# Performance work log

Hardware: AMD Instinct MI355X
Metric: run time of the kernel (lower is better)

## Reference

```python
import math
import jax, jax.numpy as jnp
import numpy as np

B, N, DIM = 2, 4096, 768
H, DK, DV = 8, 64, 64


def setup_inputs() -> dict:
    key = jax.random.key(0)
    ks = jax.random.split(key, 6)
    s = 0.02
    return {
        "x": jax.random.normal(ks[0], (B, N, DIM), dtype=jnp.float32),
        "Wq": jax.random.normal(ks[1], (DIM, H * DK), dtype=jnp.float32) * s,
        "Wk": jax.random.normal(ks[2], (DIM, H * DK), dtype=jnp.float32) * s,
        "Wv": jax.random.normal(ks[3], (DIM, H * DV), dtype=jnp.float32) * s,
        "Wo": jax.random.normal(ks[4], (H * DV, DIM), dtype=jnp.float32) * s,
        "bo": jax.random.normal(ks[5], (DIM,), dtype=jnp.float32) * s,
    }


def reference(x, Wq, Wk, Wv, Wo, bo):
    b, n, _ = x.shape
    # project and split heads: [B, H, N, d]
    q = (x @ Wq).reshape(b, n, H, DK).transpose(0, 2, 1, 3)
    k = (x @ Wk).reshape(b, n, H, DK).transpose(0, 2, 1, 3)
    v = (x @ Wv).reshape(b, n, H, DV).transpose(0, 2, 1, 3)
    scale = 1.0 / math.sqrt(DK)
    scores = jnp.einsum("bhnd,bhmd->bhnm", q, k) * scale  # [B,H,N,N]
    attn = jax.nn.softmax(scores, axis=-1)
    out = jnp.einsum("bhnm,bhmd->bhnd", attn, v)  # [B,H,N,DV]
    out = out.transpose(0, 2, 1, 3).reshape(b, n, H * DV)
    return out @ Wo + bo
```

## Files before the change

### kernel.cpp

```cpp
#include <hip/hip_runtime.h>
#include <hip/hip_bf16.h>

#define B_   2
#define N_   4096
#define DIM_ 768
#define H_   8
#define MROWS_ 8192

typedef __bf16 bf16x8 __attribute__((ext_vector_type(8)));
typedef __bf16 bf16x4 __attribute__((ext_vector_type(4)));
typedef float  f32x4  __attribute__((ext_vector_type(4)));

static __device__ __forceinline__ f32x4 mfma16(bf16x8 a, bf16x8 b, f32x4 c) {
    return __builtin_amdgcn_mfma_f32_16x16x32_bf16(a, b, c, 0, 0, 0);
}

#define GLDS16(g, l) \
    __builtin_amdgcn_global_load_lds((const __attribute__((address_space(1))) void*)(g), \
                                     (__attribute__((address_space(3))) void*)(l), 16, 0, 0)

__global__ void cvt_x_kernel(const float* __restrict__ x, __bf16* __restrict__ xb, int n4) {
    int i = blockIdx.x * blockDim.x + threadIdx.x;
    if (i >= n4) return;
    float4 f = reinterpret_cast<const float4*>(x)[i];
    bf16x4 o;
    o[0] = (__bf16)f.x; o[1] = (__bf16)f.y; o[2] = (__bf16)f.z; o[3] = (__bf16)f.w;
    reinterpret_cast<bf16x4*>(xb)[i] = o;
}

__global__ __launch_bounds__(256) void transpose_w_kernel(const float* __restrict__ Wq,
                                                          const float* __restrict__ Wk,
                                                          const float* __restrict__ Wv,
                                                          const float* __restrict__ Wo,
                                                          __bf16* __restrict__ wt,
                                                          __bf16* __restrict__ wot) {
    __shared__ float tile[64][65];
    const int bix = blockIdx.x;
    const float* src;
    int src_ld, rbase, cbase, dst_ld, drow, dcol;
    __bf16* dst;
    if (bix < 288) {
        int m = bix / 96, t = bix - m * 96;
        int tr = t >> 3, tc = t & 7;
        src = (m == 0) ? Wq : ((m == 1) ? Wk : Wv);
        src_ld = 512; rbase = tr * 64; cbase = tc * 64;
        dst = wt; dst_ld = 768; drow = m * 512 + tc * 64; dcol = tr * 64;
    } else {
        int t = bix - 288;
        int tr = t / 12, tc = t - tr * 12;
        src = Wo; src_ld = 768; rbase = tr * 64; cbase = tc * 64;
        dst = wot; dst_ld = 512; drow = tc * 64; dcol = tr * 64;
    }
#pragma unroll
    for (int kk = 0; kk < 4; ++kk) {
        int idx = threadIdx.x + kk * 256;
        int r = idx >> 4, c = (idx & 15) << 2;
        float4 f = *reinterpret_cast<const float4*>(&src[(size_t)(rbase + r) * src_ld + cbase + c]);
        tile[r][c] = f.x; tile[r][c + 1] = f.y; tile[r][c + 2] = f.z; tile[r][c + 3] = f.w;
    }
    __syncthreads();
#pragma unroll
    for (int kk = 0; kk < 4; ++kk) {
        int idx = threadIdx.x + kk * 256;
        int r = idx >> 4, c = (idx & 15) << 2;
        bf16x4 ov;
        ov[0] = (__bf16)tile[c][r];     ov[1] = (__bf16)tile[c + 1][r];
        ov[2] = (__bf16)tile[c + 2][r]; ov[3] = (__bf16)tile[c + 3][r];
        *reinterpret_cast<bf16x4*>(&dst[(size_t)(drow + r) * dst_ld + dcol + c]) = ov;
    }
}

template<int KSTEPS>
__device__ __forceinline__ void gemm_tile_main(const __bf16* __restrict__ A, const int lda,
                                               const int arow0,
                                               const __bf16* __restrict__ Bt, const int ldb,
                                               const int bcol0,
                                               __bf16* __restrict__ abuf,
                                               __bf16* __restrict__ bbuf,
                                               f32x4 (&acc)[4][4]) {
    const int lane = threadIdx.x & 63, wave = threadIdx.x >> 6;
    const int lr = lane & 15, lg = lane >> 4;
    const int wr = wave >> 1, wc = wave & 1;

    const int cid0 = wave * 128 + lane;
    const int cid1 = cid0 + 64;
    const __bf16* sA0 = A  + (size_t)(arow0 + (cid0 >> 2)) * lda + (cid0 & 3) * 8;
    const __bf16* sA1 = A  + (size_t)(arow0 + (cid1 >> 2)) * lda + (cid1 & 3) * 8;
    const __bf16* sB0 = Bt + (size_t)(bcol0 + (cid0 >> 2)) * ldb + (cid0 & 3) * 8;
    const __bf16* sB1 = Bt + (size_t)(bcol0 + (cid1 >> 2)) * ldb + (cid1 & 3) * 8;

    auto stage = [&](int buf, int ks) {
        __bf16* da = abuf + buf * 4096 + wave * 1024;
        __bf16* db = bbuf + buf * 4096 + wave * 1024;
        GLDS16(sA0 + ks * 32, da);
        GLDS16(sA1 + ks * 32, da + 512);
        GLDS16(sB0 + ks * 32, db);
        GLDS16(sB1 + ks * 32, db + 512);
    };

    stage(0, 0);
    asm volatile("s_waitcnt vmcnt(0)" ::: "memory");
    __syncthreads();

    const int ar_off = (wr * 64 + lr) * 32 + lg * 8;
    const int br_off = (wc * 64 + lr) * 32 + lg * 8;

    int buf = 0;
    for (int ks = 0; ks < KSTEPS; ++ks) {
        if (ks + 1 < KSTEPS) stage(buf ^ 1, ks + 1);
        const __bf16* ab = abuf + buf * 4096 + ar_off;
        const __bf16* bb = bbuf + buf * 4096 + br_off;
        bf16x8 af[4], bfr[4];
#pragma unroll
        for (int m = 0; m < 4; ++m) af[m] = *reinterpret_cast<const bf16x8*>(ab + m * 512);
#pragma unroll
        for (int n = 0; n < 4; ++n) bfr[n] = *reinterpret_cast<const bf16x8*>(bb + n * 512);
#pragma unroll
        for (int m = 0; m < 4; ++m)
#pragma unroll
            for (int n = 0; n < 4; ++n)
                acc[m][n] = mfma16(af[m], bfr[n], acc[m][n]);
        asm volatile("s_waitcnt vmcnt(0)" ::: "memory");
        __syncthreads();
        buf ^= 1;
    }
}

__global__ __launch_bounds__(256) void qkv_gemm_kernel(const __bf16* __restrict__ xb,
                                                       const __bf16* __restrict__ wt,
                                                       __bf16* __restrict__ q,
                                                       __bf16* __restrict__ k,
                                                       __bf16* __restrict__ vt) {
    __shared__ __align__(16) __bf16 abuf[2 * 4096];
    __shared__ __align__(16) __bf16 bbuf[2 * 4096];

    const int bid = blockIdx.x;
    const int vb = (bid & 7) * 96 + (bid >> 3);
    const int by = vb % 12, bx = vb / 12;

    f32x4 acc[4][4] = {};
    gemm_tile_main<24>(xb, 768, bx * 128, wt, 768, by * 128, abuf, bbuf, acc);

    const int lane = threadIdx.x & 63, wave = threadIdx.x >> 6;
    const int lr = lane & 15, lg = lane >> 4;
    const int wr = wave >> 1, wc = wave & 1;
    const int bi = (bx * 128) >> 12;
    const int nbase = (bx * 128) & 4095;

    const float QSCALE = 0.125f * 1.44269504089f;

#pragma unroll
    for (int n = 0; n < 4; ++n) {
        const int col0 = by * 128 + wc * 64 + n * 16;
        const int mtx = col0 >> 9;
        const int h   = (col0 >> 6) & 7;
        const int d0  = (col0 & 63) + lr;
        const size_t hb = (size_t)(bi * 8 + h);
#pragma unroll
        for (int m = 0; m < 4; ++m) {
            const int nn = nbase + wr * 64 + m * 16 + lg * 4;
            if (mtx == 0) {
#pragma unroll
                for (int r = 0; r < 4; ++r)
                    q[(hb * 4096 + nn + r) * 64 + d0] = (__bf16)(acc[m][n][r] * QSCALE);
            } else if (mtx == 1) {
#pragma unroll
                for (int r = 0; r < 4; ++r)
                    k[(hb * 4096 + nn + r) * 64 + d0] = (__bf16)acc[m][n][r];
            } else {
                bf16x4 ov;
#pragma unroll
                for (int r = 0; r < 4; ++r) ov[r] = (__bf16)acc[m][n][r];
                *reinterpret_cast<bf16x4*>(&vt[(hb * 64 + d0) * 4096 + nn]) = ov;
            }
        }
    }
}

__global__ __launch_bounds__(256) void attn_kernel(const __bf16* __restrict__ q,
                                                   const __bf16* __restrict__ k,
                                                   const __bf16* __restrict__ vt,
                                                   __bf16* __restrict__ o) {
    const int lane = threadIdx.x & 63, wave = threadIdx.x >> 6;
    const int lr = lane & 15, lg = lane >> 4;

    const int bid  = blockIdx.x;
    const int vbid = (bid & 7) * 64 + (bid >> 3);
    const int qtile = vbid & 31;
    const int bh    = vbid >> 5;
    const int qbase = qtile * 128 + wave * 32;

    const __bf16* Qh = q  + (size_t)bh * N_ * 64;
    const __bf16* Kh = k  + (size_t)bh * N_ * 64;
    const __bf16* Vh = vt + (size_t)bh * 64 * N_;

    __shared__ __align__(16) __bf16 kbuf[2][2][64][64];
    __shared__ __align__(16) __bf16 vbuf[2][2][64][64];
    __bf16* kb0 = &kbuf[0][0][0][0];
    __bf16* vb0 = &vbuf[0][0][0][0];

    const int l8 = lane >> 3, l7 = lane & 7;
    const int swz8 = (l7 ^ l8) * 8;

    int ksrc[4];
#pragma unroll
    for (int c = 0; c < 4; ++c) {
        int i = (wave & 1) * 32 + c * 8 + l8;
        int sig = ((i >> 4) & 1) * 32 + ((i >> 2) & 3) * 8 + ((i >> 5) & 1) * 4 + (i & 3);
        ksrc[c] = sig * 64 + swz8;
    }

    auto stageK1 = [&](__bf16* dstbase, int jt) {
        if (wave < 2) {
            const __bf16* srcb = Kh + (size_t)jt * 4096;
            __bf16* dst = dstbase + (wave & 1) * 2048;
#pragma unroll
            for (int c = 0; c < 4; ++c)
                GLDS16(srcb + ksrc[c], dst + c * 512);
        }
    };
    auto stageV1 = [&](__bf16* dstbase, int jt) {
        if (wave >= 2) {
            const int w2 = wave - 2;
            const __bf16* src = Vh + (size_t)(w2 * 32 + l8) * 4096 + jt * 64 + swz8;
            __bf16* dst = dstbase + w2 * 2048;
#pragma unroll
            for (int c = 0; c < 4; ++c)
                GLDS16(src + (size_t)c * 8 * 4096, dst + c * 512);
        }
    };

    bf16x8 qf[2][2];
#pragma unroll
    for (int frag = 0; frag < 2; ++frag)
#pragma unroll
        for (int kc = 0; kc < 2; ++kc)
            qf[frag][kc] = *reinterpret_cast<const bf16x8*>(
                Qh + (size_t)(qbase + frag * 16 + lr) * 64 + kc * 32 + lg * 8);

    f32x4 acc[2][4] = {};
    f32x4 accl[2] = {};
    bf16x8 vones;
#pragma unroll
    for (int t = 0; t < 8; ++t) vones[t] = (__bf16)1.0f;

    auto QK = [&](f32x4 (&s)[2][4], const __bf16* kb_) {
        const char* kb = (const char*)kb_;
        __builtin_amdgcn_s_setprio(1);
#pragma unroll
        for (int kc = 0; kc < 2; ++kc) {
#pragma unroll
            for (int cb = 0; cb < 4; ++cb) {
                const int row = cb * 16 + lr;
                bf16x8 bk = *reinterpret_cast<const bf16x8*>(
                    kb + row * 128 + (((kc * 4 + lg) ^ (lr & 7)) << 4));
                if (kc == 0) { s[0][cb] = mfma16(bk, qf[0][0], {}); s[1][cb] = mfma16(bk, qf[1][0], {}); }
                else         { s[0][cb] = mfma16(bk, qf[0][1], s[0][cb]); s[1][cb] = mfma16(bk, qf[1][1], s[1][cb]); }
            }
        }
        __builtin_amdgcn_s_setprio(0);
    };
    auto EXP = [&](f32x4 (&s)[2][4], bf16x8 (&pk)[2][2]) {
#pragma unroll
        for (int frag = 0; frag < 2; ++frag)
#pragma unroll
            for (int kc = 0; kc < 2; ++kc) {
#pragma unroll
                for (int t = 0; t < 8; ++t)
                    pk[frag][kc][t] = (__bf16)__builtin_amdgcn_exp2f(s[frag][kc + 2 * (t >> 2)][t & 3]);
                accl[frag] = mfma16(pk[frag][kc], vones, accl[frag]);
            }
    };
    auto PV = [&](bf16x8 (&pk)[2][2], const __bf16* vb_) {
        const char* vb = (const char*)vb_;
        __builtin_amdgcn_s_setprio(1);
#pragma unroll
        for (int kc = 0; kc < 2; ++kc) {
#pragma unroll
            for (int cbv = 0; cbv < 4; ++cbv) {
                const int row = cbv * 16 + lr;
                bf16x8 bv = *reinterpret_cast<const bf16x8*>(
                    vb + row * 128 + (((kc * 4 + lg) ^ (lr & 7)) << 4));
                acc[0][cbv] = mfma16(pk[0][kc], bv, acc[0][cbv]);
                acc[1][cbv] = mfma16(pk[1][kc], bv, acc[1][cbv]);
            }
        }
        __builtin_amdgcn_s_setprio(0);
    };

    f32x4 sA[2][4], sB[2][4];
    bf16x8 pkA[2][2], pkB[2][2];

    int rdo = 8192, wro = 0;

    stageK1(kb0 + 8192, 0);
    stageK1(kb0 + 8192 + 4096, 1);
    stageV1(vb0 + 8192 + 4096, 0);
    asm volatile("s_waitcnt vmcnt(0)" ::: "memory");
    __builtin_amdgcn_s_barrier();

    stageK1(kb0 + wro, 2);          stageK1(kb0 + wro + 4096, 3);
    stageV1(vb0 + wro, 1);          stageV1(vb0 + wro + 4096, 2);
    QK(sB, kb0 + rdo);
    EXP(sB, pkB);
    QK(sA, kb0 + rdo + 4096);
    PV(pkB, vb0 + rdo + 4096);
    asm volatile("s_waitcnt vmcnt(0)" ::: "memory");
    __builtin_amdgcn_s_barrier();
    rdo ^= 8192; wro ^= 8192;

    for (int P = 1; P <= 30; ++P) {
        const int a = 2 * P;
        stageK1(kb0 + wro, a + 2);      stageK1(kb0 + wro + 4096, a + 3);
        stageV1(vb0 + wro, a + 1);      stageV1(vb0 + wro + 4096, a + 2);
        EXP(sA, pkA);
        QK(sB, kb0 + rdo);
        PV(pkA, vb0 + rdo);
        EXP(sB, pkB);
        QK(sA, kb0 + rdo + 4096);
        PV(pkB, vb0 + rdo + 4096);
        asm volatile("s_waitcnt vmcnt(0)" ::: "memory");
        __builtin_amdgcn_s_barrier();
        rdo ^= 8192; wro ^= 8192;
    }

    stageV1(vb0 + wro, 63);
    EXP(sA, pkA);
    QK(sB, kb0 + rdo);
    PV(pkA, vb0 + rdo);
    EXP(sB, pkB);
    QK(sA, kb0 + rdo + 4096);
    PV(pkB, vb0 + rdo + 4096);
    asm volatile("s_waitcnt vmcnt(0)" ::: "memory");
    __builtin_amdgcn_s_barrier();

    EXP(sA, pkA);
    PV(pkA, vb0 + wro);

    const int b = bh >> 3, h = bh & 7;
#pragma unroll
    for (int frag = 0; frag < 2; ++frag) {
#pragma unroll
        for (int r = 0; r < 4; ++r) {
            float inv = 1.f / accl[frag][r];
            int row = b * N_ + qbase + frag * 16 + lg * 4 + r;
#pragma unroll
            for (int cbv = 0; cbv < 4; ++cbv)
                o[(size_t)row * 512 + h * 64 + cbv * 16 + lr] =
                    (__bf16)(acc[frag][cbv][r] * inv);
        }
    }
}

__global__ __launch_bounds__(256) void out_gemm_kernel(const __bf16* __restrict__ ob,
                                                       const __bf16* __restrict__ wot,
                                                       const float* __restrict__ bo,
                                                       float* __restrict__ out) {
    __shared__ __align__(16) __bf16 abuf[2 * 4096];
    __shared__ __align__(16) __bf16 bbuf[2 * 4096];

    const int bid = blockIdx.x;
    const int vb = (bid & 7) * 48 + (bid >> 3);
    const int by = vb % 6, bx = vb / 6;

    f32x4 acc[4][4] = {};
    gemm_tile_main<16>(ob, 512, bx * 128, wot, 512, by * 128, abuf, bbuf, acc);

    const int lane = threadIdx.x & 63, wave = threadIdx.x >> 6;
    const int lr = lane & 15, lg = lane >> 4;
    const int wr = wave >> 1, wc = wave & 1;

#pragma unroll
    for (int n = 0; n < 4; ++n) {
        const int col = by * 128 + wc * 64 + n * 16 + lr;
        const float bias = bo[col];
#pragma unroll
        for (int m = 0; m < 4; ++m) {
            const int row0 = bx * 128 + wr * 64 + m * 16 + lg * 4;
#pragma unroll
            for (int r = 0; r < 4; ++r)
                out[(size_t)(row0 + r) * 768 + col] = acc[m][n][r] + bias;
        }
    }
}

extern "C" void kernel_launch(void* const* d_in, const int* in_sizes, int n_in,
                              void* d_out, int out_size, void* d_ws, size_t ws_size,
                              hipStream_t stream) {
    const float* x  = (const float*)d_in[0];
    const float* Wq = (const float*)d_in[1];
    const float* Wk = (const float*)d_in[2];
    const float* Wv = (const float*)d_in[3];
    const float* Wo = (const float*)d_in[4];
    const float* bo = (const float*)d_in[5];
    float* out = (float*)d_out;

    char* ws = (char*)d_ws;
    __bf16* xb  = (__bf16*)(ws);
    __bf16* wt  = (__bf16*)(ws + 12582912);
    __bf16* wot = (__bf16*)(ws + 12582912 + 2359296);
    char*   p0  = ws + 12582912 + 2359296 + 786432;
    __bf16* qw  = (__bf16*)(p0);
    __bf16* kw  = (__bf16*)(p0 + 8388608);
    __bf16* vtw = (__bf16*)(p0 + 2 * (size_t)8388608);
    __bf16* obf = (__bf16*)(p0 + 3 * (size_t)8388608);

    cvt_x_kernel<<<6144, 256, 0, stream>>>(x, xb, MROWS_ * DIM_ / 4);
    transpose_w_kernel<<<384, 256, 0, stream>>>(Wq, Wk, Wv, Wo, wt, wot);
    qkv_gemm_kernel<<<768, 256, 0, stream>>>(xb, wt, qw, kw, vtw);
    attn_kernel<<<512, 256, 0, stream>>>(qw, kw, vtw, obf);
    out_gemm_kernel<<<384, 256, 0, stream>>>(obf, wot, bo, out);
}
```

Before: 128.8 us.

## Double attention query tile per block and drop software-pipelined score buffers

Result: slower. 146.0 us (+13.4%).

```diff
diff --git a/kernel.cpp b/kernel.cpp
--- a/kernel.cpp
+++ b/kernel.cpp
@@ -177,18 +177,18 @@
     }
 }
 
-__global__ __launch_bounds__(256) void attn_kernel(const __bf16* __restrict__ q,
-                                                   const __bf16* __restrict__ k,
-                                                   const __bf16* __restrict__ vt,
-                                                   __bf16* __restrict__ o) {
+__global__ __launch_bounds__(256, 1) void attn_kernel(const __bf16* __restrict__ q,
+                                                      const __bf16* __restrict__ k,
+                                                      const __bf16* __restrict__ vt,
+                                                      __bf16* __restrict__ o) {
     const int lane = threadIdx.x & 63, wave = threadIdx.x >> 6;
     const int lr = lane & 15, lg = lane >> 4;
 
     const int bid  = blockIdx.x;
-    const int vbid = (bid & 7) * 64 + (bid >> 3);
-    const int qtile = vbid & 31;
-    const int bh    = vbid >> 5;
-    const int qbase = qtile * 128 + wave * 32;
+    const int vbid = (bid & 7) * 32 + (bid >> 3);
+    const int qtile = vbid & 15;
+    const int bh    = vbid >> 4;
+    const int qbase = qtile * 256 + wave * 64;
 
     const __bf16* Qh = q  + (size_t)bh * N_ * 64;
     const __bf16* Kh = k  + (size_t)bh * N_ * 64;
@@ -230,21 +230,24 @@
         }
     };
 
-    bf16x8 qf[2][2];
-#pragma unroll
-    for (int frag = 0; frag < 2; ++frag)
+    bf16x8 qf[4][2];
+#pragma unroll
+    for (int frag = 0; frag < 4; ++frag)
 #pragma unroll
         for (int kc = 0; kc < 2; ++kc)
             qf[frag][kc] = *reinterpret_cast<const bf16x8*>(
                 Qh + (size_t)(qbase + frag * 16 + lr) * 64 + kc * 32 + lg * 8);
 
-    f32x4 acc[2][4] = {};
-    f32x4 accl[2] = {};
+    f32x4 acc[4][4] = {};
+    f32x4 accl[4] = {};
     bf16x8 vones;
 #pragma unroll
     for (int t = 0; t < 8; ++t) vones[t] = (__bf16)1.0f;
 
-    auto QK = [&](f32x4 (&s)[2][4], const __bf16* kb_) {
+    f32x4 s[4][4];
+    bf16x8 pk[4][2];
+
+    auto QK = [&](const __bf16* kb_) {
         const char* kb = (const char*)kb_;
         __builtin_amdgcn_s_setprio(1);
 #pragma unroll
@@ -254,15 +257,18 @@
                 const int row = cb * 16 + lr;
                 bf16x8 bk = *reinterpret_cast<const bf16x8*>(
                     kb + row * 128 + (((kc * 4 + lg) ^ (lr & 7)) << 4));
-                if (kc == 0) { s[0][cb] = mfma16(bk, qf[0][0], {}); s[1][cb] = mfma16(bk, qf[1][0], {}); }
-                else         { s[0][cb] = mfma16(bk, qf[0][1], s[0][cb]); s[1][cb] = mfma16(bk, qf[1][1], s[1][cb]); }
+#pragma unroll
+                for (int frag = 0; frag < 4; ++frag) {
+                    if (kc == 0) s[frag][cb] = mfma16(bk, qf[frag][0], {});
+                    else         s[frag][cb] = mfma16(bk, qf[frag][1], s[frag][cb]);
+                }
             }
         }
         __builtin_amdgcn_s_setprio(0);
     };
-    auto EXP = [&](f32x4 (&s)[2][4], bf16x8 (&pk)[2][2]) {
-#pragma unroll
-        for (int frag = 0; frag < 2; ++frag)
+    auto EXP = [&]() {
+#pragma unroll
+        for (int frag = 0; frag < 4; ++frag)
 #pragma unroll
             for (int kc = 0; kc < 2; ++kc) {
 #pragma unroll
@@ -271,7 +277,7 @@
                 accl[frag] = mfma16(pk[frag][kc], vones, accl[frag]);
             }
     };
-    auto PV = [&](bf16x8 (&pk)[2][2], const __bf16* vb_) {
+    auto PV = [&](const __bf16* vb_) {
         const char* vb = (const char*)vb_;
         __builtin_amdgcn_s_setprio(1);
 #pragma unroll
@@ -281,15 +287,13 @@
                 const int row = cbv * 16 + lr;
                 bf16x8 bv = *reinterpret_cast<const bf16x8*>(
                     vb + row * 128 + (((kc * 4 + lg) ^ (lr & 7)) << 4));
-                acc[0][cbv] = mfma16(pk[0][kc], bv, acc[0][cbv]);
-                acc[1][cbv] = mfma16(pk[1][kc], bv, acc[1][cbv]);
+#pragma unroll
+                for (int frag = 0; frag < 4; ++frag)
+                    acc[frag][cbv] = mfma16(pk[frag][kc], bv, acc[frag][cbv]);
             }
         }
         __builtin_amdgcn_s_setprio(0);
     };
-
-    f32x4 sA[2][4], sB[2][4];
-    bf16x8 pkA[2][2], pkB[2][2];
 
     int rdo = 8192, wro = 0;
 
@@ -301,10 +305,11 @@
 
     stageK1(kb0 + wro, 2);          stageK1(kb0 + wro + 4096, 3);
     stageV1(vb0 + wro, 1);          stageV1(vb0 + wro + 4096, 2);
-    QK(sB, kb0 + rdo);
-    EXP(sB, pkB);
-    QK(sA, kb0 + rdo + 4096);
-    PV(pkB, vb0 + rdo + 4096);
+    QK(kb0 + rdo);
+    EXP();
+    QK(kb0 + rdo + 4096);
+    PV(vb0 + rdo + 4096);
+    EXP();
     asm volatile("s_waitcnt vmcnt(0)" ::: "memory");
     __builtin_amdgcn_s_barrier();
     rdo ^= 8192; wro ^= 8192;
@@ -313,33 +318,32 @@
         const int a = 2 * P;
         stageK1(kb0 + wro, a + 2);      stageK1(kb0 + wro + 4096, a + 3);
         stageV1(vb0 + wro, a + 1);      stageV1(vb0 + wro + 4096, a + 2);
-        EXP(sA, pkA);
-        QK(sB, kb0 + rdo);
-        PV(pkA, vb0 + rdo);
-        EXP(sB, pkB);
-        QK(sA, kb0 + rdo + 4096);
-        PV(pkB, vb0 + rdo + 4096);
+        QK(kb0 + rdo);
+        PV(vb0 + rdo);
+        EXP();
+        QK(kb0 + rdo + 4096);
+        PV(vb0 + rdo + 4096);
+        EXP();
         asm volatile("s_waitcnt vmcnt(0)" ::: "memory");
         __builtin_amdgcn_s_barrier();
         rdo ^= 8192; wro ^= 8192;
     }
 
     stageV1(vb0 + wro, 63);
-    EXP(sA, pkA);
-    QK(sB, kb0 + rdo);
-    PV(pkA, vb0 + rdo);
-    EXP(sB, pkB);
-    QK(sA, kb0 + rdo + 4096);
-    PV(pkB, vb0 + rdo + 4096);
+    QK(kb0 + rdo);
+    PV(vb0 + rdo);
+    EXP();
+    QK(kb0 + rdo + 4096);
+    PV(vb0 + rdo + 4096);
+    EXP();
     asm volatile("s_waitcnt vmcnt(0)" ::: "memory");
     __builtin_amdgcn_s_barrier();
 
-    EXP(sA, pkA);
-    PV(pkA, vb0 + wro);
+    PV(vb0 + wro);
 
     const int b = bh >> 3, h = bh & 7;
 #pragma unroll
-    for (int frag = 0; frag < 2; ++frag) {
+    for (int frag = 0; frag < 4; ++frag) {
 #pragma unroll
         for (int r = 0; r < 4; ++r) {
             float inv = 1.f / accl[frag][r];
@@ -408,6 +412,6 @@
     cvt_x_kernel<<<6144, 256, 0, stream>>>(x, xb, MROWS_ * DIM_ / 4);
     transpose_w_kernel<<<384, 256, 0, stream>>>(Wq, Wk, Wv, Wo, wt, wot);
     qkv_gemm_kernel<<<768, 256, 0, stream>>>(xb, wt, qw, kw, vtw);
-    attn_kernel<<<512, 256, 0, stream>>>(qw, kw, vtw, obf);
+    attn_kernel<<<256, 256, 0, stream>>>(qw, kw, vtw, obf);
     out_gemm_kernel<<<384, 256, 0, stream>>>(obf, wot, bo, out);
 }
```
